# Optimization experiments

Hardware: AMD Instinct MI355X
Metric: run time of the kernel (lower is better)

Reference implementation:

```python
import jax, jax.numpy as jnp
import numpy as np

B, L, E, Q = 32, 2048, 512, 512

def setup_inputs() -> dict:
    key = jax.random.key(0)
    k1, k2, k3, k4, k5 = jax.random.split(key, 5)
    scale_attn = 1.0 / np.sqrt(E + Q)
    scale_v = 1.0 / np.sqrt(E)
    return {
        "embeddings": jax.random.normal(k1, (B, L, E), dtype=jnp.float32),
        "query": jax.random.normal(k2, (B, L, Q), dtype=jnp.float32),
        "W_attn": jax.random.normal(k3, (E, E + Q), dtype=jnp.float32) * scale_attn,
        "b_attn": jax.random.normal(k4, (E,), dtype=jnp.float32) * scale_attn,
        "v_w": jax.random.normal(k5, (E,), dtype=jnp.float32) * scale_v,
    }

def reference(embeddings, query, W_attn, b_attn, v_w):
    # concat along feature dim: (B, L, Q+E)
    cat = jnp.concatenate([query, embeddings], axis=2)
    # attn_layer: Linear(E+Q -> E), then tanh: (B, L, E)
    h = jnp.tanh(jnp.einsum('blf,ef->ble', cat, W_attn) + b_attn)
    # attn_v: Linear(E -> 1, no bias) -> scores (B, L)
    scores = jnp.einsum('ble,e->bl', h, v_w)
    # softmax over the sequence (dim=1 in torch)
    w = jax.nn.softmax(scores, axis=1)  # (B, L)
    # transpose to (B, 1, L) then bmm with embeddings -> (B, 1, E)
    applied = jnp.einsum('bl,ble->be', w, embeddings)[:, None, :]
    weights = w[:, None, :]
    return (applied, weights)
```

## Files before the change

### kernel.cpp

```cpp
#include <hip/hip_runtime.h>
#include <hip/hip_bf16.h>
#include <math.h>


typedef __attribute__((ext_vector_type(8))) short bf16x8;
typedef __attribute__((ext_vector_type(4))) float f32x4;

#define BDIM 32
#define LDIM 2048
#define EDIM 512
#define QDIM 512
#define KDIM 1024
#define MDIM (BDIM * LDIM)

#define BM 128
#define BN 128
#define BK 64
#define LDS_STRIDE (BK + 8)

__device__ inline unsigned short f2bf(float x) {
    unsigned int u = __builtin_bit_cast(unsigned int, x);
    u += 0x7FFF + ((u >> 16) & 1);
    return (unsigned short)(u >> 16);
}

__global__ __launch_bounds__(256) void scores_kernel(
    const float* __restrict__ emb, const float* __restrict__ query,
    const float* __restrict__ W, const float* __restrict__ b_attn,
    const float* __restrict__ v_w, float* __restrict__ scores)
{
    __shared__ unsigned short As[BM][LDS_STRIDE];
    __shared__ unsigned short Bs[BN][LDS_STRIDE];

    const int tid = threadIdx.x;
    const int bid = blockIdx.x;
    const int mtile = bid >> 2;
    const int ntile = bid & 3;
    const int m0 = mtile * BM;
    const int n0 = ntile * BN;

    const int lane = tid & 63;
    const int wv = tid >> 6;
    const int wm = (wv >> 1) * 64;
    const int wn = (wv & 1) * 64;
    const int quad = lane >> 4;
    const int ln = lane & 15;

    const int row16 = tid >> 4;
    const int col4  = (tid & 15) * 4;

    f32x4 acc[4][4];
    #pragma unroll
    for (int i = 0; i < 4; i++)
        #pragma unroll
        for (int j = 0; j < 4; j++)
            acc[i][j] = (f32x4){0.f, 0.f, 0.f, 0.f};

    for (int k0 = 0; k0 < KDIM; k0 += BK) {
        const float* asrc = (k0 < QDIM) ? query : emb;
        const int koff = (k0 < QDIM) ? k0 : (k0 - QDIM);
        #pragma unroll
        for (int p = 0; p < 8; p++) {
            const int r = p * 16 + row16;
            const float4 v = *(const float4*)(asrc + (size_t)(m0 + r) * 512 + koff + col4);
            ushort4 pk;
            pk.x = f2bf(v.x); pk.y = f2bf(v.y); pk.z = f2bf(v.z); pk.w = f2bf(v.w);
            *(ushort4*)&As[r][col4] = pk;
        }
        #pragma unroll
        for (int p = 0; p < 8; p++) {
            const int r = p * 16 + row16;
            const float4 v = *(const float4*)(W + (size_t)(n0 + r) * 1024 + k0 + col4);
            ushort4 pk;
            pk.x = f2bf(v.x); pk.y = f2bf(v.y); pk.z = f2bf(v.z); pk.w = f2bf(v.w);
            *(ushort4*)&Bs[r][col4] = pk;
        }
        __syncthreads();

        #pragma unroll
        for (int ks = 0; ks < 2; ks++) {
            bf16x8 af[4], bf[4];
            #pragma unroll
            for (int i = 0; i < 4; i++)
                af[i] = *(const bf16x8*)&As[wm + i * 16 + ln][ks * 32 + quad * 8];
            #pragma unroll
            for (int j = 0; j < 4; j++)
                bf[j] = *(const bf16x8*)&Bs[wn + j * 16 + ln][ks * 32 + quad * 8];
            #pragma unroll
            for (int i = 0; i < 4; i++)
                #pragma unroll
                for (int j = 0; j < 4; j++)
                    acc[i][j] = __builtin_amdgcn_mfma_f32_16x16x32_bf16(af[i], bf[j], acc[i][j], 0, 0, 0);
        }
        __syncthreads();
    }

    float bj[4], vj[4];
    #pragma unroll
    for (int j = 0; j < 4; j++) {
        const int n = n0 + wn + j * 16 + ln;
        bj[j] = b_attn[n];
        vj[j] = v_w[n];
    }
    #pragma unroll
    for (int i = 0; i < 4; i++) {
        #pragma unroll
        for (int r = 0; r < 4; r++) {
            float s = 0.f;
            #pragma unroll
            for (int j = 0; j < 4; j++)
                s += tanhf(acc[i][j][r] + bj[j]) * vj[j];
            #pragma unroll
            for (int off = 1; off < 16; off <<= 1)
                s += __shfl_xor(s, off, 64);
            if (ln == 0)
                atomicAdd(&scores[m0 + wm + i * 16 + quad * 4 + r], s);
        }
    }
}

__global__ __launch_bounds__(256) void softmax_apply_kernel(
    const float* __restrict__ emb, const float* __restrict__ scores,
    float* __restrict__ out_applied, float* __restrict__ out_weights)
{
    const int b = blockIdx.x >> 4;
    const int chunk = blockIdx.x & 15;
    const int l0 = chunk * 128;
    const int tid = threadIdx.x;
    const float* srow = scores + b * LDIM;

    __shared__ float red[4];
    __shared__ float wls[128];

    float mx = -1e30f;
    #pragma unroll
    for (int t = 0; t < 8; t++) mx = fmaxf(mx, srow[tid + t * 256]);
    #pragma unroll
    for (int off = 1; off < 64; off <<= 1) mx = fmaxf(mx, __shfl_xor(mx, off, 64));
    if ((tid & 63) == 0) red[tid >> 6] = mx;
    __syncthreads();
    mx = fmaxf(fmaxf(red[0], red[1]), fmaxf(red[2], red[3]));

    float sm = 0.f;
    #pragma unroll
    for (int t = 0; t < 8; t++) sm += expf(srow[tid + t * 256] - mx);
    #pragma unroll
    for (int off = 1; off < 64; off <<= 1) sm += __shfl_xor(sm, off, 64);
    __syncthreads();
    if ((tid & 63) == 0) red[tid >> 6] = sm;
    __syncthreads();
    sm = red[0] + red[1] + red[2] + red[3];
    const float inv = 1.f / sm;

    if (tid < 128) {
        const float w = expf(srow[l0 + tid] - mx) * inv;
        wls[tid] = w;
        out_weights[(size_t)b * LDIM + l0 + tid] = w;
    }
    __syncthreads();

    float2 acc = {0.f, 0.f};
    const float2* erow = (const float2*)(emb + ((size_t)b * LDIM + l0) * EDIM);
    for (int l = 0; l < 128; l++) {
        const float2 v = erow[(size_t)l * 256 + tid];
        const float w = wls[l];
        acc.x += w * v.x;
        acc.y += w * v.y;
    }
    atomicAdd(&out_applied[b * EDIM + 2 * tid], acc.x);
    atomicAdd(&out_applied[b * EDIM + 2 * tid + 1], acc.y);
}

extern "C" void kernel_launch(void* const* d_in, const int* in_sizes, int n_in,
                              void* d_out, int out_size, void* d_ws, size_t ws_size,
                              hipStream_t stream) {
    const float* emb    = (const float*)d_in[0];
    const float* query  = (const float*)d_in[1];
    const float* W      = (const float*)d_in[2];
    const float* b_attn = (const float*)d_in[3];
    const float* v_w    = (const float*)d_in[4];

    float* out     = (float*)d_out;
    float* applied = out;
    float* weights = out + BDIM * EDIM;
    float* scores  = (float*)d_ws;

    hipMemsetAsync(scores, 0, (size_t)MDIM * sizeof(float), stream);
    hipMemsetAsync(applied, 0, (size_t)BDIM * EDIM * sizeof(float), stream);

    scores_kernel<<<2048, 256, 0, stream>>>(emb, query, W, b_attn, v_w, scores);

    softmax_apply_kernel<<<512, 256, 0, stream>>>(emb, scores, applied, weights);
}
```

Baseline: 413.7 us.

## Cheapen bf16 packing, remap blocks per XCD, and widen softmax-apply loads

Replaces round-to-nearest-even bf16 conversion with add-and-perm packing of two floats per instruction, cutting ALU work in the GEMM staging loop, though rounding ties now go away from zero instead of to even. Remaps block IDs so each XCD handles a contiguous range of M tiles, improving L2 reuse of the A rows shared by the four N tiles. The softmax/apply kernel uses twice as many blocks with 64 rows each, float4 loads, and an in-block reduction of two halves before the atomics, raising memory-level parallelism for the embedding read.

```diff
diff --git a/kernel.cpp b/kernel.cpp
--- a/kernel.cpp
+++ b/kernel.cpp
@@ -18,10 +18,10 @@
 #define BK 64
 #define LDS_STRIDE (BK + 8)
 
-__device__ inline unsigned short f2bf(float x) {
-    unsigned int u = __builtin_bit_cast(unsigned int, x);
-    u += 0x7FFF + ((u >> 16) & 1);
-    return (unsigned short)(u >> 16);
+__device__ inline unsigned int pack2bf(float lo, float hi) {
+    unsigned int a = __builtin_bit_cast(unsigned int, lo) + 0x8000u;
+    unsigned int b = __builtin_bit_cast(unsigned int, hi) + 0x8000u;
+    return __builtin_amdgcn_perm(b, a, 0x07060302);
 }
 
 __global__ __launch_bounds__(256) void scores_kernel(
@@ -34,8 +34,10 @@
 
     const int tid = threadIdx.x;
     const int bid = blockIdx.x;
-    const int mtile = bid >> 2;
-    const int ntile = bid & 3;
+    const int xcd = bid & 7;
+    const int slot = bid >> 3;
+    const int mtile = xcd * 64 + (slot >> 2);
+    const int ntile = slot & 3;
     const int m0 = mtile * BM;
     const int n0 = ntile * BN;
 
@@ -63,17 +65,19 @@
         for (int p = 0; p < 8; p++) {
             const int r = p * 16 + row16;
             const float4 v = *(const float4*)(asrc + (size_t)(m0 + r) * 512 + koff + col4);
-            ushort4 pk;
-            pk.x = f2bf(v.x); pk.y = f2bf(v.y); pk.z = f2bf(v.z); pk.w = f2bf(v.w);
-            *(ushort4*)&As[r][col4] = pk;
+            uint2 pk;
+            pk.x = pack2bf(v.x, v.y);
+            pk.y = pack2bf(v.z, v.w);
+            *(uint2*)&As[r][col4] = pk;
         }
         #pragma unroll
         for (int p = 0; p < 8; p++) {
             const int r = p * 16 + row16;
             const float4 v = *(const float4*)(W + (size_t)(n0 + r) * 1024 + k0 + col4);
-            ushort4 pk;
-            pk.x = f2bf(v.x); pk.y = f2bf(v.y); pk.z = f2bf(v.z); pk.w = f2bf(v.w);
-            *(ushort4*)&Bs[r][col4] = pk;
+            uint2 pk;
+            pk.x = pack2bf(v.x, v.y);
+            pk.y = pack2bf(v.z, v.w);
+            *(uint2*)&Bs[r][col4] = pk;
         }
         __syncthreads();
 
@@ -123,14 +127,15 @@
     const float* __restrict__ emb, const float* __restrict__ scores,
     float* __restrict__ out_applied, float* __restrict__ out_weights)
 {
-    const int b = blockIdx.x >> 4;
-    const int chunk = blockIdx.x & 15;
-    const int l0 = chunk * 128;
+    const int b = blockIdx.x >> 5;
+    const int chunk = blockIdx.x & 31;
+    const int l0 = chunk * 64;
     const int tid = threadIdx.x;
     const float* srow = scores + b * LDIM;
 
     __shared__ float red[4];
-    __shared__ float wls[128];
+    __shared__ float wls[64];
+    __shared__ float partial[128 * 4];
 
     float mx = -1e30f;
     #pragma unroll
@@ -152,23 +157,36 @@
     sm = red[0] + red[1] + red[2] + red[3];
     const float inv = 1.f / sm;
 
-    if (tid < 128) {
+    if (tid < 64) {
         const float w = expf(srow[l0 + tid] - mx) * inv;
         wls[tid] = w;
         out_weights[(size_t)b * LDIM + l0 + tid] = w;
     }
     __syncthreads();
 
-    float2 acc = {0.f, 0.f};
-    const float2* erow = (const float2*)(emb + ((size_t)b * LDIM + l0) * EDIM);
-    for (int l = 0; l < 128; l++) {
-        const float2 v = erow[(size_t)l * 256 + tid];
-        const float w = wls[l];
+    const int half = tid >> 7;
+    const int cg = tid & 127;
+    float4 acc = {0.f, 0.f, 0.f, 0.f};
+    const float* ebase = emb + ((size_t)b * LDIM + l0 + half) * EDIM + cg * 4;
+    #pragma unroll 8
+    for (int i = 0; i < 32; i++) {
+        const float4 v = *(const float4*)(ebase + (size_t)2 * i * EDIM);
+        const float w = wls[half + 2 * i];
         acc.x += w * v.x;
         acc.y += w * v.y;
-    }
-    atomicAdd(&out_applied[b * EDIM + 2 * tid], acc.x);
-    atomicAdd(&out_applied[b * EDIM + 2 * tid + 1], acc.y);
+        acc.z += w * v.z;
+        acc.w += w * v.w;
+    }
+    if (half == 1) *(float4*)&partial[cg * 4] = acc;
+    __syncthreads();
+    if (half == 0) {
+        const float4 p = *(const float4*)&partial[cg * 4];
+        float* dst = out_applied + b * EDIM + cg * 4;
+        atomicAdd(dst + 0, acc.x + p.x);
+        atomicAdd(dst + 1, acc.y + p.y);
+        atomicAdd(dst + 2, acc.z + p.z);
+        atomicAdd(dst + 3, acc.w + p.w);
+    }
 }
 
 extern "C" void kernel_launch(void* const* d_in, const int* in_sizes, int n_in,
@@ -190,5 +208,5 @@
 
     scores_kernel<<<2048, 256, 0, stream>>>(emb, query, W, b_attn, v_w, scores);
 
-    softmax_apply_kernel<<<512, 256, 0, stream>>>(emb, scores, applied, weights);
-}
+    softmax_apply_kernel<<<1024, 256, 0, stream>>>(emb, scores, applied, weights);
+}
```

New measurement: 406.2 us. Within noise of the previous version (-1.8%).
